# Optimization experiments

Hardware: AMD Instinct MI355X
Metric: run time of the kernel (lower is better)

The kernel has to match this reference:

```python
import jax, jax.numpy as jnp
import numpy as np

LEVELS = 16
FEATURES = 2
TABLE_SIZE = 2 ** 19
MINRES = (16, 16)
MAXRES = (2048, 2048)
N = 2 ** 21  # number of query points
PRIMES = (1, 2654435761)  # Instant-NGP spatial hash primes (2D)


def _level_res():
    # per-dim geometric growth: floor(minres * b**l), b = exp((ln(max)-ln(min))/(L-1))
    res = []
    for l in range(LEVELS):
        r = []
        for mn, mx in zip(MINRES, MAXRES):
            b = np.exp((np.log(mx) - np.log(mn)) / (LEVELS - 1))
            r.append(int(np.floor(mn * b ** l)))
        res.append(tuple(r))
    return res


RES_LEVELS = _level_res()


def setup_inputs() -> dict:
    key = jax.random.key(0)
    k1, k2, k3, k4 = jax.random.split(key, 4)
    coords_x = jax.random.uniform(k1, (N,), jnp.float32)
    coords_y = jax.random.uniform(k2, (N,), jnp.float32)
    # level 0 is a dense grid table; levels 1..L-1 are hash tables (stacked)
    dense_table = jax.random.uniform(k3, (*RES_LEVELS[0], FEATURES), jnp.float32, -1e-4, 1e-4)
    hash_tables = jax.random.uniform(k4, (LEVELS - 1, TABLE_SIZE, FEATURES), jnp.float32, -1e-4, 1e-4)
    return {"coords_x": coords_x, "coords_y": coords_y,
            "dense_table": dense_table, "hash_tables": hash_tables}


def _bilerp(gather, res, cx, cy):
    # normalized coords in [0,1] scaled to index space [0, res-1]; mode='nearest' -> clamp
    rx, ry = res
    fx = cx * (rx - 1)
    fy = cy * (ry - 1)
    x0 = jnp.floor(fx)
    y0 = jnp.floor(fy)
    wx = (fx - x0)[:, None]
    wy = (fy - y0)[:, None]
    ix0 = jnp.clip(x0.astype(jnp.int32), 0, rx - 1)
    iy0 = jnp.clip(y0.astype(jnp.int32), 0, ry - 1)
    ix1 = jnp.minimum(ix0 + 1, rx - 1)
    iy1 = jnp.minimum(iy0 + 1, ry - 1)
    f00 = gather(ix0, iy0)  # [N, F]
    f01 = gather(ix0, iy1)
    f10 = gather(ix1, iy0)
    f11 = gather(ix1, iy1)
    return (f00 * (1 - wx) * (1 - wy) + f01 * (1 - wx) * wy
            + f10 * wx * (1 - wy) + f11 * wx * wy)


def _hash_gather(table, ix, iy):
    h = (ix.astype(jnp.uint32) * jnp.uint32(PRIMES[0])) ^ (iy.astype(jnp.uint32) * jnp.uint32(PRIMES[1]))
    idx = (h % jnp.uint32(table.shape[0])).astype(jnp.int32)
    return table[idx]


def reference(coords_x, coords_y, dense_table, hash_tables):
    feats = [_bilerp(lambda ix, iy: dense_table[ix, iy], RES_LEVELS[0], coords_x, coords_y)]
    for l in range(1, LEVELS):
        t = hash_tables[l - 1]
        feats.append(_bilerp(lambda ix, iy, t=t: _hash_gather(t, ix, iy),
                             RES_LEVELS[l], coords_x, coords_y))
    return jnp.concatenate(feats, -1)  # [N, LEVELS*FEATURES]
```

## Files before the change

### kernel.cpp

```cpp
#include <hip/hip_runtime.h>
#include <math.h>
#include <stdint.h>


#define TMASK  ((1u << 19) - 1)
#define PRIME2 2654435761u

typedef float vfloat4 __attribute__((ext_vector_type(4)));
typedef float vfloat2 __attribute__((ext_vector_type(2)));

__global__ __launch_bounds__(256, 8) void mre_big(
    const float* __restrict__ cxp, const float* __restrict__ cyp,
    const float2* __restrict__ hasht, vfloat2* __restrict__ ws,
    uint4 rm1v, unsigned N)
{
    unsigned bid = blockIdx.x;
    unsigned xcd = bid & 7u;
    unsigned lv  = xcd >> 1;
    unsigned bwl = (bid >> 3) * 2u + (xcd & 1u);
    int r = (int)(lv == 0u ? rm1v.x : lv == 1u ? rm1v.y
                                    : lv == 2u ? rm1v.z : rm1v.w);
    const char* hb = (const char*)hasht + ((size_t)(11u + lv) << 22);
    vfloat2* wbase = ws + (size_t)lv * N;
    float rf = (float)r;

    unsigned stride = 512u * 256u;
    #pragma unroll 2
    for (unsigned n = bwl * 256u + threadIdx.x; n < N; n += stride) {
        float x = cxp[n], y = cyp[n];
        float fx = x * rf, fy = y * rf;
        float x0f = floorf(fx), y0f = floorf(fy);
        float wx = fx - x0f, wy = fy - y0f;
        int ix0 = (int)x0f; ix0 = ix0 < 0 ? 0 : (ix0 > r ? r : ix0);
        int iy0 = (int)y0f; iy0 = iy0 < 0 ? 0 : (iy0 > r ? r : iy0);
        int ix1 = ix0 + 1 > r ? r : ix0 + 1;
        int iy1 = iy0 + 1 > r ? r : iy0 + 1;
        unsigned hy0 = (unsigned)iy0 * PRIME2;
        unsigned hy1 = (unsigned)iy1 * PRIME2;
        float2 f00 = *(const float2*)(hb + ((((unsigned)ix0 ^ hy0) & TMASK) << 3));
        float2 f01 = *(const float2*)(hb + ((((unsigned)ix0 ^ hy1) & TMASK) << 3));
        float2 f10 = *(const float2*)(hb + ((((unsigned)ix1 ^ hy0) & TMASK) << 3));
        float2 f11 = *(const float2*)(hb + ((((unsigned)ix1 ^ hy1) & TMASK) << 3));
        float omx = 1.0f - wx, omy = 1.0f - wy;
        float w00 = omx * omy, w01 = omx * wy, w10 = wx * omy, w11 = wx * wy;
        vfloat2 acc;
        acc.x = f00.x * w00 + f01.x * w01 + f10.x * w10 + f11.x * w11;
        acc.y = f00.y * w00 + f01.y * w01 + f10.y * w10 + f11.y * w11;
        __builtin_nontemporal_store(acc, wbase + n);
    }
}

__global__ __launch_bounds__(256) void mre_rest(
    const float* __restrict__ cxp, const float* __restrict__ cyp,
    const float2* __restrict__ dense, const float2* __restrict__ hasht,
    const vfloat2* __restrict__ ws, float4* __restrict__ out,
    uint4 wa, uint4 wb, unsigned N)
{
    __shared__ float2 sdense[256];
    sdense[threadIdx.x] = dense[threadIdx.x];
    __syncthreads();

    unsigned gid = blockIdx.x * 256u + threadIdx.x;
    unsigned n = gid >> 2;
    unsigned j = gid & 3u;

    float x = cxp[n];
    float y = cyp[n];

    float2 acc[4];
    if (j == 3u) {
        #pragma unroll
        for (int k = 0; k < 4; ++k) {
            vfloat2 v = ws[(size_t)k * N + n];
            acc[k].x = v.x; acc[k].y = v.y;
        }
    } else {
        unsigned w0 = j == 0u ? wa.x : (j == 1u ? wa.z : wb.x);
        unsigned w1 = j == 0u ? wa.y : (j == 1u ? wa.w : wb.y);
        int rm1[4] = { (int)(w0 & 0xffffu), (int)(w0 >> 16),
                       (int)(w1 & 0xffffu), (int)(w1 >> 16) };

        unsigned o00[4], o01[4], o10[4], o11[4];
        float wx[4], wy[4];
        unsigned d00 = 0, d01 = 0, d10 = 0, d11 = 0;
        const bool lvl0 = (j == 0u);

        #pragma unroll
        for (int k = 0; k < 4; ++k) {
            int r = rm1[k];
            float rf = (float)r;
            float fx = x * rf, fy = y * rf;
            float x0f = floorf(fx), y0f = floorf(fy);
            wx[k] = fx - x0f;  wy[k] = fy - y0f;
            int ix0 = (int)x0f; ix0 = ix0 < 0 ? 0 : (ix0 > r ? r : ix0);
            int iy0 = (int)y0f; iy0 = iy0 < 0 ? 0 : (iy0 > r ? r : iy0);
            int ix1 = ix0 + 1 > r ? r : ix0 + 1;
            int iy1 = iy0 + 1 > r ? r : iy0 + 1;
            if (k == 0) { d00 = ix0 * 16 + iy0; d01 = ix0 * 16 + iy1;
                          d10 = ix1 * 16 + iy0; d11 = ix1 * 16 + iy1; }
            unsigned ti = j * 4u + (unsigned)k;
            ti = ti == 0u ? 0u : ti - 1u;
            unsigned tb = ti << 22;
            unsigned hy0 = (unsigned)iy0 * PRIME2;
            unsigned hy1 = (unsigned)iy1 * PRIME2;
            o00[k] = tb + ((((unsigned)ix0 ^ hy0) & TMASK) << 3);
            o01[k] = tb + ((((unsigned)ix0 ^ hy1) & TMASK) << 3);
            o10[k] = tb + ((((unsigned)ix1 ^ hy0) & TMASK) << 3);
            o11[k] = tb + ((((unsigned)ix1 ^ hy1) & TMASK) << 3);
        }

        const char* hb = (const char*)hasht;
        float2 f00[4], f01[4], f10[4], f11[4];
        #pragma unroll
        for (int k = 1; k < 4; ++k) {
            f00[k] = *(const float2*)(hb + o00[k]);
            f01[k] = *(const float2*)(hb + o01[k]);
            f10[k] = *(const float2*)(hb + o10[k]);
            f11[k] = *(const float2*)(hb + o11[k]);
        }
        if (lvl0) {
            f00[0] = sdense[d00]; f01[0] = sdense[d01];
            f10[0] = sdense[d10]; f11[0] = sdense[d11];
        } else {
            f00[0] = *(const float2*)(hb + o00[0]);
            f01[0] = *(const float2*)(hb + o01[0]);
            f10[0] = *(const float2*)(hb + o10[0]);
            f11[0] = *(const float2*)(hb + o11[0]);
        }

        #pragma unroll
        for (int k = 0; k < 4; ++k) {
            float omx = 1.0f - wx[k], omy = 1.0f - wy[k];
            float w00 = omx * omy, w01 = omx * wy[k];
            float w10 = wx[k] * omy, w11 = wx[k] * wy[k];
            acc[k].x = f00[k].x * w00 + f01[k].x * w01 + f10[k].x * w10 + f11[k].x * w11;
            acc[k].y = f00[k].y * w00 + f01[k].y * w01 + f10[k].y * w10 + f11[k].y * w11;
        }
    }

    vfloat4 o0 = { acc[0].x, acc[0].y, acc[1].x, acc[1].y };
    vfloat4 o1 = { acc[2].x, acc[2].y, acc[3].x, acc[3].y };
    size_t base = (size_t)n * 8u + 2u * j;
    __builtin_nontemporal_store(o0, (vfloat4*)&out[base]);
    __builtin_nontemporal_store(o1, (vfloat4*)&out[base + 1]);
}

__global__ __launch_bounds__(256) void mre_mono(
    const float* __restrict__ cxp, const float* __restrict__ cyp,
    const float2* __restrict__ dense, const float2* __restrict__ hasht,
    float4* __restrict__ out, uint4 wa, uint4 wb)
{
    __shared__ float2 sdense[256];
    sdense[threadIdx.x] = dense[threadIdx.x];
    __syncthreads();

    unsigned gid = blockIdx.x * 256u + threadIdx.x;
    unsigned n = gid >> 2;
    unsigned j = gid & 3u;

    float x = cxp[n];
    float y = cyp[n];

    unsigned w0 = j < 2u ? (j == 0u ? wa.x : wa.z) : (j == 2u ? wb.x : wb.z);
    unsigned w1 = j < 2u ? (j == 0u ? wa.y : wa.w) : (j == 2u ? wb.y : wb.w);
    int rm1[4] = { (int)(w0 & 0xffffu), (int)(w0 >> 16),
                   (int)(w1 & 0xffffu), (int)(w1 >> 16) };

    unsigned o00[4], o01[4], o10[4], o11[4];
    float wx[4], wy[4];
    unsigned d00 = 0, d01 = 0, d10 = 0, d11 = 0;
    const bool lvl0 = (j == 0u);

    #pragma unroll
    for (int k = 0; k < 4; ++k) {
        int r = rm1[k];
        float rf = (float)r;
        float fx = x * rf, fy = y * rf;
        float x0f = floorf(fx), y0f = floorf(fy);
        wx[k] = fx - x0f;  wy[k] = fy - y0f;
        int ix0 = (int)x0f; ix0 = ix0 < 0 ? 0 : (ix0 > r ? r : ix0);
        int iy0 = (int)y0f; iy0 = iy0 < 0 ? 0 : (iy0 > r ? r : iy0);
        int ix1 = ix0 + 1 > r ? r : ix0 + 1;
        int iy1 = iy0 + 1 > r ? r : iy0 + 1;
        if (k == 0) { d00 = ix0 * 16 + iy0; d01 = ix0 * 16 + iy1;
                      d10 = ix1 * 16 + iy0; d11 = ix1 * 16 + iy1; }
        unsigned ti = j * 4u + (unsigned)k;
        ti = ti == 0u ? 0u : ti - 1u;
        unsigned tb = ti << 22;
        unsigned hy0 = (unsigned)iy0 * PRIME2;
        unsigned hy1 = (unsigned)iy1 * PRIME2;
        o00[k] = tb + ((((unsigned)ix0 ^ hy0) & TMASK) << 3);
        o01[k] = tb + ((((unsigned)ix0 ^ hy1) & TMASK) << 3);
        o10[k] = tb + ((((unsigned)ix1 ^ hy0) & TMASK) << 3);
        o11[k] = tb + ((((unsigned)ix1 ^ hy1) & TMASK) << 3);
    }

    const char* hb = (const char*)hasht;
    float2 f00[4], f01[4], f10[4], f11[4];
    #pragma unroll
    for (int k = 1; k < 4; ++k) {
        f00[k] = *(const float2*)(hb + o00[k]);
        f01[k] = *(const float2*)(hb + o01[k]);
        f10[k] = *(const float2*)(hb + o10[k]);
        f11[k] = *(const float2*)(hb + o11[k]);
    }
    if (lvl0) {
        f00[0] = sdense[d00]; f01[0] = sdense[d01];
        f10[0] = sdense[d10]; f11[0] = sdense[d11];
    } else {
        f00[0] = *(const float2*)(hb + o00[0]);
        f01[0] = *(const float2*)(hb + o01[0]);
        f10[0] = *(const float2*)(hb + o10[0]);
        f11[0] = *(const float2*)(hb + o11[0]);
    }

    float2 acc[4];
    #pragma unroll
    for (int k = 0; k < 4; ++k) {
        float omx = 1.0f - wx[k], omy = 1.0f - wy[k];
        float w00 = omx * omy, w01 = omx * wy[k];
        float w10 = wx[k] * omy, w11 = wx[k] * wy[k];
        acc[k].x = f00[k].x * w00 + f01[k].x * w01 + f10[k].x * w10 + f11[k].x * w11;
        acc[k].y = f00[k].y * w00 + f01[k].y * w01 + f10[k].y * w10 + f11[k].y * w11;
    }

    vfloat4 o0 = { acc[0].x, acc[0].y, acc[1].x, acc[1].y };
    vfloat4 o1 = { acc[2].x, acc[2].y, acc[3].x, acc[3].y };
    size_t base = (size_t)n * 8u + 2u * j;
    __builtin_nontemporal_store(o0, (vfloat4*)&out[base]);
    __builtin_nontemporal_store(o1, (vfloat4*)&out[base + 1]);
}

extern "C" void kernel_launch(void* const* d_in, const int* in_sizes, int n_in,
                              void* d_out, int out_size, void* d_ws, size_t ws_size,
                              hipStream_t stream)
{
    const float*  cx    = (const float*)d_in[0];
    const float*  cy    = (const float*)d_in[1];
    const float2* dense = (const float2*)d_in[2];
    const float2* hasht = (const float2*)d_in[3];
    float4*       out   = (float4*)d_out;
    const unsigned N = (unsigned)in_sizes[0];

    int r[16];
    for (int l = 0; l < 16; ++l) {
        double b = exp((log(2048.0) - log(16.0)) / 15.0);
        r[l] = (int)floor(16.0 * pow(b, (double)l));
    }
    unsigned pw[8];
    for (int k = 0; k < 8; ++k)
        pw[k] = (unsigned)(r[2 * k] - 1) | ((unsigned)(r[2 * k + 1] - 1) << 16);
    uint4 wa = make_uint4(pw[0], pw[1], pw[2], pw[3]);
    uint4 wb = make_uint4(pw[4], pw[5], pw[6], pw[7]);

    long long total = (long long)N * 4;
    int blocks = (int)((total + 255) / 256);

    size_t ws_need = (size_t)4 * N * sizeof(float2);
    if (ws_size >= ws_need && d_ws != nullptr) {
        uint4 rm1v = make_uint4((unsigned)(r[12] - 1), (unsigned)(r[13] - 1),
                                (unsigned)(r[14] - 1), (unsigned)(r[15] - 1));
        vfloat2* ws = (vfloat2*)d_ws;
        hipLaunchKernelGGL(mre_big, dim3(2048), dim3(256), 0, stream,
                           cx, cy, hasht, ws, rm1v, N);
        hipLaunchKernelGGL(mre_rest, dim3(blocks), dim3(256), 0, stream,
                           cx, cy, dense, hasht, (const vfloat2*)ws, out, wa, wb, N);
    } else {
        hipLaunchKernelGGL(mre_mono, dim3(blocks), dim3(256), 0, stream,
                           cx, cy, dense, hasht, out, wa, wb);
    }
}
```

Measured before the change: 706.8 us.

## Balance rest-kernel lanes to three levels each and transpose outputs via LDS

```diff
diff --git a/kernel.cpp b/kernel.cpp
--- a/kernel.cpp
+++ b/kernel.cpp
@@ -57,89 +57,96 @@
     uint4 wa, uint4 wb, unsigned N)
 {
     __shared__ float2 sdense[256];
+    __shared__ __align__(16) float sout[64 * 36];
     sdense[threadIdx.x] = dense[threadIdx.x];
     __syncthreads();
 
     unsigned gid = blockIdx.x * 256u + threadIdx.x;
-    unsigned n = gid >> 2;
-    unsigned j = gid & 3u;
+    unsigned n  = gid >> 2;
+    unsigned j  = gid & 3u;
+    unsigned nl = threadIdx.x >> 2;
 
     float x = cxp[n];
     float y = cyp[n];
 
-    float2 acc[4];
-    if (j == 3u) {
-        #pragma unroll
-        for (int k = 0; k < 4; ++k) {
-            vfloat2 v = ws[(size_t)k * N + n];
-            acc[k].x = v.x; acc[k].y = v.y;
-        }
+    vfloat2 wsv = __builtin_nontemporal_load(&ws[(size_t)j * N + n]);
+
+    unsigned W0 = wa.x, W1 = wa.y, W2 = wa.z, W3 = wa.w, W4 = wb.x, W5 = wb.y;
+    unsigned u0 = j == 0u ? W0 : j == 1u ? W1 : j == 2u ? W3 : W4;
+    unsigned u1 = j == 0u ? W0 : j == 1u ? W2 : j == 2u ? W3 : W5;
+    unsigned u2 = j == 0u ? W1 : j == 1u ? W2 : j == 2u ? W4 : W5;
+    unsigned h0 = (j & 1u) << 4;
+    unsigned h1 = ((j + 1u) & 1u) << 4;
+    unsigned h2 = (j & 1u) << 4;
+    int rm1[3] = { (int)((u0 >> h0) & 0xffffu),
+                   (int)((u1 >> h1) & 0xffffu),
+                   (int)((u2 >> h2) & 0xffffu) };
+
+    unsigned o00[3], o01[3], o10[3], o11[3];
+    float wx[3], wy[3];
+    unsigned d00 = 0, d01 = 0, d10 = 0, d11 = 0;
+
+    #pragma unroll
+    for (int k = 0; k < 3; ++k) {
+        int r = rm1[k];
+        float rf = (float)r;
+        float fx = x * rf, fy = y * rf;
+        float x0f = floorf(fx), y0f = floorf(fy);
+        wx[k] = fx - x0f;  wy[k] = fy - y0f;
+        int ix0 = (int)x0f; ix0 = ix0 < 0 ? 0 : (ix0 > r ? r : ix0);
+        int iy0 = (int)y0f; iy0 = iy0 < 0 ? 0 : (iy0 > r ? r : iy0);
+        int ix1 = ix0 + 1 > r ? r : ix0 + 1;
+        int iy1 = iy0 + 1 > r ? r : iy0 + 1;
+        if (k == 0) { d00 = ix0 * 16 + iy0; d01 = ix0 * 16 + iy1;
+                      d10 = ix1 * 16 + iy0; d11 = ix1 * 16 + iy1; }
+        unsigned lvl = j * 3u + (unsigned)k;
+        unsigned ti = lvl == 0u ? 0u : lvl - 1u;
+        unsigned tb = ti << 22;
+        unsigned hy0 = (unsigned)iy0 * PRIME2;
+        unsigned hy1 = (unsigned)iy1 * PRIME2;
+        o00[k] = tb + ((((unsigned)ix0 ^ hy0) & TMASK) << 3);
+        o01[k] = tb + ((((unsigned)ix0 ^ hy1) & TMASK) << 3);
+        o10[k] = tb + ((((unsigned)ix1 ^ hy0) & TMASK) << 3);
+        o11[k] = tb + ((((unsigned)ix1 ^ hy1) & TMASK) << 3);
+    }
+
+    const char* hb = (const char*)hasht;
+    float2 f00[3], f01[3], f10[3], f11[3];
+    #pragma unroll
+    for (int k = 1; k < 3; ++k) {
+        f00[k] = *(const float2*)(hb + o00[k]);
+        f01[k] = *(const float2*)(hb + o01[k]);
+        f10[k] = *(const float2*)(hb + o10[k]);
+        f11[k] = *(const float2*)(hb + o11[k]);
+    }
+    if (j == 0u) {
+        f00[0] = sdense[d00]; f01[0] = sdense[d01];
+        f10[0] = sdense[d10]; f11[0] = sdense[d11];
     } else {
-        unsigned w0 = j == 0u ? wa.x : (j == 1u ? wa.z : wb.x);
-        unsigned w1 = j == 0u ? wa.y : (j == 1u ? wa.w : wb.y);
-        int rm1[4] = { (int)(w0 & 0xffffu), (int)(w0 >> 16),
-                       (int)(w1 & 0xffffu), (int)(w1 >> 16) };
-
-        unsigned o00[4], o01[4], o10[4], o11[4];
-        float wx[4], wy[4];
-        unsigned d00 = 0, d01 = 0, d10 = 0, d11 = 0;
-        const bool lvl0 = (j == 0u);
-
-        #pragma unroll
-        for (int k = 0; k < 4; ++k) {
-            int r = rm1[k];
-            float rf = (float)r;
-            float fx = x * rf, fy = y * rf;
-            float x0f = floorf(fx), y0f = floorf(fy);
-            wx[k] = fx - x0f;  wy[k] = fy - y0f;
-            int ix0 = (int)x0f; ix0 = ix0 < 0 ? 0 : (ix0 > r ? r : ix0);
-            int iy0 = (int)y0f; iy0 = iy0 < 0 ? 0 : (iy0 > r ? r : iy0);
-            int ix1 = ix0 + 1 > r ? r : ix0 + 1;
-            int iy1 = iy0 + 1 > r ? r : iy0 + 1;
-            if (k == 0) { d00 = ix0 * 16 + iy0; d01 = ix0 * 16 + iy1;
-                          d10 = ix1 * 16 + iy0; d11 = ix1 * 16 + iy1; }
-            unsigned ti = j * 4u + (unsigned)k;
-            ti = ti == 0u ? 0u : ti - 1u;
-            unsigned tb = ti << 22;
-            unsigned hy0 = (unsigned)iy0 * PRIME2;
-            unsigned hy1 = (unsigned)iy1 * PRIME2;
-            o00[k] = tb + ((((unsigned)ix0 ^ hy0) & TMASK) << 3);
-            o01[k] = tb + ((((unsigned)ix0 ^ hy1) & TMASK) << 3);
-            o10[k] = tb + ((((unsigned)ix1 ^ hy0) & TMASK) << 3);
-            o11[k] = tb + ((((unsigned)ix1 ^ hy1) & TMASK) << 3);
-        }
-
-        const char* hb = (const char*)hasht;
-        float2 f00[4], f01[4], f10[4], f11[4];
-        #pragma unroll
-        for (int k = 1; k < 4; ++k) {
-            f00[k] = *(const float2*)(hb + o00[k]);
-            f01[k] = *(const float2*)(hb + o01[k]);
-            f10[k] = *(const float2*)(hb + o10[k]);
-            f11[k] = *(const float2*)(hb + o11[k]);
-        }
-        if (lvl0) {
-            f00[0] = sdense[d00]; f01[0] = sdense[d01];
-            f10[0] = sdense[d10]; f11[0] = sdense[d11];
-        } else {
-            f00[0] = *(const float2*)(hb + o00[0]);
-            f01[0] = *(const float2*)(hb + o01[0]);
-            f10[0] = *(const float2*)(hb + o10[0]);
-            f11[0] = *(const float2*)(hb + o11[0]);
-        }
-
-        #pragma unroll
-        for (int k = 0; k < 4; ++k) {
-            float omx = 1.0f - wx[k], omy = 1.0f - wy[k];
-            float w00 = omx * omy, w01 = omx * wy[k];
-            float w10 = wx[k] * omy, w11 = wx[k] * wy[k];
-            acc[k].x = f00[k].x * w00 + f01[k].x * w01 + f10[k].x * w10 + f11[k].x * w11;
-            acc[k].y = f00[k].y * w00 + f01[k].y * w01 + f10[k].y * w10 + f11[k].y * w11;
-        }
-    }
-
-    vfloat4 o0 = { acc[0].x, acc[0].y, acc[1].x, acc[1].y };
-    vfloat4 o1 = { acc[2].x, acc[2].y, acc[3].x, acc[3].y };
+        f00[0] = *(const float2*)(hb + o00[0]);
+        f01[0] = *(const float2*)(hb + o01[0]);
+        f10[0] = *(const float2*)(hb + o10[0]);
+        f11[0] = *(const float2*)(hb + o11[0]);
+    }
+
+    float* so = &sout[nl * 36u];
+    #pragma unroll
+    for (int k = 0; k < 3; ++k) {
+        float omx = 1.0f - wx[k], omy = 1.0f - wy[k];
+        float w00 = omx * omy, w01 = omx * wy[k];
+        float w10 = wx[k] * omy, w11 = wx[k] * wy[k];
+        vfloat2 a;
+        a.x = f00[k].x * w00 + f01[k].x * w01 + f10[k].x * w10 + f11[k].x * w11;
+        a.y = f00[k].y * w00 + f01[k].y * w01 + f10[k].y * w10 + f11[k].y * w11;
+        *(vfloat2*)&so[6u * j + 2u * (unsigned)k] = a;
+    }
+    *(vfloat2*)&so[24u + 2u * j] = wsv;
+
+    __syncthreads();
+
+    const vfloat4* sp = (const vfloat4*)&sout[nl * 36u + 8u * j];
+    vfloat4 o0 = sp[0];
+    vfloat4 o1 = sp[1];
     size_t base = (size_t)n * 8u + 2u * j;
     __builtin_nontemporal_store(o0, (vfloat4*)&out[base]);
     __builtin_nontemporal_store(o1, (vfloat4*)&out[base + 1]);
```

New measurement: 673.0 us. 1.05x faster.
